# Optimization experiments

Hardware: AMD Instinct MI355X
Metric: run time of the kernel (lower is better)

Reference implementation:

```python
import jax, jax.numpy as jnp
import numpy as np

B, S, D, H = 2, 2048, 512, 8
HD = D // H  # head_size = 64
EPS = 1e-5


def _layer_norm(x, g, b):
    m = jnp.mean(x, axis=-1, keepdims=True)
    v = jnp.mean(jnp.square(x - m), axis=-1, keepdims=True)
    return (x - m) * jax.lax.rsqrt(v + EPS) * g + b


def setup_inputs() -> dict:
    key = jax.random.key(0)
    ks = jax.random.split(key, 16)
    s_in = 1.0 / np.sqrt(D)
    s_ff = 1.0 / np.sqrt(4 * D)
    return {
        "x": jax.random.normal(ks[0], (B, S, D), jnp.float32),
        # per-head q/k/v projections stacked over heads: [H, D, HD]
        "Wq": jax.random.normal(ks[1], (H, D, HD), jnp.float32) * s_in,
        "bq": jax.random.normal(ks[2], (H, HD), jnp.float32) * s_in,
        "Wk": jax.random.normal(ks[3], (H, D, HD), jnp.float32) * s_in,
        "bk": jax.random.normal(ks[4], (H, HD), jnp.float32) * s_in,
        "Wv": jax.random.normal(ks[5], (H, D, HD), jnp.float32) * s_in,
        "bv": jax.random.normal(ks[6], (H, HD), jnp.float32) * s_in,
        "Wp": jax.random.normal(ks[7], (D, D), jnp.float32) * s_in,
        "bp": jax.random.normal(ks[8], (D,), jnp.float32) * s_in,
        "W1": jax.random.normal(ks[9], (D, 4 * D), jnp.float32) * s_in,
        "b1": jax.random.normal(ks[10], (4 * D,), jnp.float32) * s_in,
        "W2": jax.random.normal(ks[11], (4 * D, D), jnp.float32) * s_ff,
        "b2": jax.random.normal(ks[12], (D,), jnp.float32) * s_ff,
        "g1": jnp.ones((D,), jnp.float32),
        "be1": jnp.zeros((D,), jnp.float32),
        "g2": jnp.ones((D,), jnp.float32),
        "be2": jnp.zeros((D,), jnp.float32),
    }


def reference(x, Wq, bq, Wk, bk, Wv, bv, Wp, bp, W1, b1, W2, b2, g1, be1, g2, be2):
    # --- attention sublayer (pre-norm) ---
    xn = _layer_norm(x, g1, be1)                               # [B,S,D]
    q = jnp.einsum('bsd,hde->bhse', xn, Wq) + bq[None, :, None, :]
    k = jnp.einsum('bsd,hde->bhse', xn, Wk) + bk[None, :, None, :]
    v = jnp.einsum('bsd,hde->bhse', xn, Wv) + bv[None, :, None, :]
    # NOTE: original has NO 1/sqrt(head_size) scaling and NO mask
    scores = jnp.einsum('bhse,bhte->bhst', q, k)               # [B,H,S,S]
    w = jax.nn.softmax(scores, axis=-1)
    o = jnp.einsum('bhst,bhte->bhse', w, v)                    # [B,H,S,HD]
    o = o.transpose(0, 2, 1, 3).reshape(x.shape[0], x.shape[1], D)  # concat heads
    attn_out = o @ Wp + bp
    x = x + attn_out
    # --- MLP sublayer (pre-norm) ---
    xn2 = _layer_norm(x, g2, be2)
    h = jax.nn.relu(xn2 @ W1 + b1)
    x = x + (h @ W2 + b2)
    return x
```

## Files before the change

kernel.cpp:

```cpp
#include <hip/hip_runtime.h>
#include <hip/hip_bf16.h>

typedef unsigned short u16;
typedef unsigned long long u64t;
typedef __attribute__((ext_vector_type(8))) short bhalf8;
typedef __attribute__((ext_vector_type(4))) short bhalf4;
typedef __attribute__((ext_vector_type(4))) float f32x4;

#define MFMA16(a, b, c) __builtin_amdgcn_mfma_f32_16x16x32_bf16((a), (b), (c), 0, 0, 0)

#if __has_builtin(__builtin_amdgcn_mfma_f32_16x16x16bf16_1k)
#define HAVE_K16 1
#define MFMAK16(a, b, c) __builtin_amdgcn_mfma_f32_16x16x16bf16_1k((a), (b), (c), 0, 0, 0)
#elif __has_builtin(__builtin_amdgcn_mfma_f32_16x16x16_bf16)
#define HAVE_K16 1
#define MFMAK16(a, b, c) __builtin_amdgcn_mfma_f32_16x16x16_bf16((a), (b), (c), 0, 0, 0)
#else
#define HAVE_K16 0
#endif

#if __has_builtin(__builtin_amdgcn_perm)
#define HAVE_PERM 1
#else
#define HAVE_PERM 0
#endif

#define BB 2
#define SS 2048
#define DD 512
#define HH 8
#define HD 64
#define NT (BB * SS)
#define LOG2E 1.44269504f

#if __has_builtin(__builtin_amdgcn_exp2f)
#define EXP2(x) __builtin_amdgcn_exp2f(x)
#else
#define EXP2(x) exp2f(x)
#endif

__device__ __forceinline__ u16 f2b(float f) {
    unsigned u = __builtin_bit_cast(unsigned, f);
    unsigned r = (u + 0x7fffu + ((u >> 16) & 1u)) >> 16;
    return (u16)r;
}

__device__ __forceinline__ unsigned pk2bf(float f0, float f1) {
#if HAVE_PERM
    unsigned a0 = __builtin_bit_cast(unsigned, f0) + 0x8000u;
    unsigned a1 = __builtin_bit_cast(unsigned, f1) + 0x8000u;
    return __builtin_amdgcn_perm(a1, a0, 0x07060302u);
#else
    return (unsigned)f2b(f0) | ((unsigned)f2b(f1) << 16);
#endif
}

__device__ __forceinline__ void gl2lds16(const u16* g, u16* l) {
    u16* gn = (u16*)g;
    __builtin_amdgcn_global_load_lds((__attribute__((address_space(1))) void*)gn,
                                     (__attribute__((address_space(3))) void*)l, 16, 0, 0);
}

__global__ __launch_bounds__(256) void k_prep(const float* __restrict__ Wq, const float* __restrict__ Wk,
                                              const float* __restrict__ Wv, const float* __restrict__ Wp,
                                              const float* __restrict__ W1, const float* __restrict__ W2,
                                              const float* __restrict__ bq, const float* __restrict__ bk,
                                              const float* __restrict__ bv,
                                              u16* __restrict__ WqkvT, u16* __restrict__ WpT,
                                              u16* __restrict__ W1T, u16* __restrict__ W2T,
                                              float* __restrict__ biasqkv,
                                              const float* __restrict__ x, const float* __restrict__ g1,
                                              const float* __restrict__ be1, u16* __restrict__ xn) {
    int j = blockIdx.x;
    int t = threadIdx.x;
    if (j >= 3078) {
        int wave = t >> 6, lane = t & 63;
        int row = (j - 3078) * 4 + wave;
        const float* xr = x + (size_t)row * DD;
        int c = lane * 8;
        float4 v0 = *(const float4*)(xr + c);
        float4 v1 = *(const float4*)(xr + c + 4);
        float s  = v0.x + v0.y + v0.z + v0.w + v1.x + v1.y + v1.z + v1.w;
        float sq = v0.x*v0.x + v0.y*v0.y + v0.z*v0.z + v0.w*v0.w
                 + v1.x*v1.x + v1.y*v1.y + v1.z*v1.z + v1.w*v1.w;
#pragma unroll
        for (int m = 1; m < 64; m <<= 1) {
            s  += __shfl_xor(s, m);
            sq += __shfl_xor(sq, m);
        }
        float mean = s * (1.0f / DD);
        float var  = sq * (1.0f / DD) - mean * mean;
        float rstd = rsqrtf(var + 1e-5f);
        float4 g0 = *(const float4*)(g1 + c);
        float4 g4 = *(const float4*)(g1 + c + 4);
        float4 b0 = *(const float4*)(be1 + c);
        float4 b4 = *(const float4*)(be1 + c + 4);
        float xv[8] = {v0.x, v0.y, v0.z, v0.w, v1.x, v1.y, v1.z, v1.w};
        float gv[8] = {g0.x, g0.y, g0.z, g0.w, g4.x, g4.y, g4.z, g4.w};
        float bv2[8] = {b0.x, b0.y, b0.z, b0.w, b4.x, b4.y, b4.z, b4.w};
        union { bhalf8 v; u16 u[8]; } pk;
#pragma unroll
        for (int i = 0; i < 8; i++) pk.u[i] = f2b((xv[i] - mean) * rstd * gv[i] + bv2[i]);
        *(bhalf8*)(xn + (size_t)row * DD + c) = pk.v;
        return;
    }
    int tx = t & 31, ty = t >> 5;
    if (j >= 3072) {
        int i = (j - 3072) * 256 + ty * 32 + tx;
        biasqkv[i] = (i < 512) ? bq[i] : (i < 1024) ? bk[i - 512] : bv[i - 1024];
        return;
    }
    __shared__ float tile[32][33];
    const float* src; u16* dst; int R, C, tr, tc;
    if (j < 768) {
        int m = j >> 8, rem = j & 255, h = rem >> 5, tl = rem & 31;
        tr = tl >> 1; tc = tl & 1;
        src = (m == 0 ? Wq : (m == 1 ? Wk : Wv)) + h * 32768;
        dst = WqkvT + m * 262144 + h * 32768;
        R = 512; C = 64;
    } else if (j < 1024) { int tl = j - 768;  tr = tl >> 4; tc = tl & 15; src = Wp; dst = WpT; R = 512;  C = 512;  }
    else if (j < 2048)   { int tl = j - 1024; tr = tl >> 6; tc = tl & 63; src = W1; dst = W1T; R = 512;  C = 2048; }
    else                 { int tl = j - 2048; tr = tl >> 4; tc = tl & 15; src = W2; dst = W2T; R = 2048; C = 512;  }
    int c = tc * 32 + tx;
#pragma unroll
    for (int i = 0; i < 4; i++)
        tile[ty + i * 8][tx] = src[(size_t)(tr * 32 + ty + i * 8) * C + c];
    __syncthreads();
    int r2 = tr * 32 + tx;
#pragma unroll
    for (int i = 0; i < 4; i++)
        dst[(size_t)(tc * 32 + ty + i * 8) * R + r2] = f2b(tile[tx][ty + i * 8]);
}

__global__ __launch_bounds__(256) void k_layernorm(const float* __restrict__ x,
                                                   const float* __restrict__ g,
                                                   const float* __restrict__ be,
                                                   u16* __restrict__ out) {
    int wave = threadIdx.x >> 6, lane = threadIdx.x & 63;
    int row = blockIdx.x * 4 + wave;
    const float* xr = x + (size_t)row * DD;
    int c = lane * 8;
    float4 v0 = *(const float4*)(xr + c);
    float4 v1 = *(const float4*)(xr + c + 4);
    float s  = v0.x + v0.y + v0.z + v0.w + v1.x + v1.y + v1.z + v1.w;
    float sq = v0.x*v0.x + v0.y*v0.y + v0.z*v0.z + v0.w*v0.w
             + v1.x*v1.x + v1.y*v1.y + v1.z*v1.z + v1.w*v1.w;
#pragma unroll
    for (int m = 1; m < 64; m <<= 1) {
        s  += __shfl_xor(s, m);
        sq += __shfl_xor(sq, m);
    }
    float mean = s * (1.0f / DD);
    float var  = sq * (1.0f / DD) - mean * mean;
    float rstd = rsqrtf(var + 1e-5f);
    float4 g0 = *(const float4*)(g + c);
    float4 g1 = *(const float4*)(g + c + 4);
    float4 b0 = *(const float4*)(be + c);
    float4 b1 = *(const float4*)(be + c + 4);
    float xv[8] = {v0.x, v0.y, v0.z, v0.w, v1.x, v1.y, v1.z, v1.w};
    float gv[8] = {g0.x, g0.y, g0.z, g0.w, g1.x, g1.y, g1.z, g1.w};
    float bv[8] = {b0.x, b0.y, b0.z, b0.w, b1.x, b1.y, b1.z, b1.w};
    union { bhalf8 v; u16 u[8]; } pk;
#pragma unroll
    for (int i = 0; i < 8; i++) pk.u[i] = f2b((xv[i] - mean) * rstd * gv[i] + bv[i]);
    *(bhalf8*)(out + (size_t)row * DD + c) = pk.v;
}

template<int BM, int BN, int WR, int WC, int MI, int NI, int MODE>
__global__ __launch_bounds__(256) void k_gemm(const u16* __restrict__ A, const u16* __restrict__ Bt,
                                              const float* __restrict__ bias,
                                              int lda, int ldb, int kLen, int N,
                                              const float* __restrict__ resid,
                                              float* __restrict__ outF, u16* __restrict__ outB,
                                              u16* __restrict__ qd, u16* __restrict__ kd,
                                              u16* __restrict__ vtd) {
    constexpr int WM = MI * 16;
    constexpr int WN = NI * 16;
    static_assert(WR * WM == BM && WC * WN == BN && WR * WC == 4, "cfg");
    constexpr int ACH = BM / 32;
    constexpr int BCH = BN / 32;
    __shared__ u16 As0[BM * 64];
    __shared__ u16 Bs0[BN * 64];
    __shared__ u16 As1[BM * 64];
    __shared__ u16 Bs1[BN * 64];
    int t = threadIdx.x;
    int wave = t >> 6, lane = t & 63, quad = lane >> 4, l16 = lane & 15;
    int wr, wc;
    if (WC == 1)      { wr = wave; wc = 0; }
    else if (WR == 1) { wr = 0;    wc = wave; }
    else              { wr = wave >> 1; wc = wave & 1; }
    int m0 = blockIdx.y * BM, n0 = blockIdx.x * BN;

    f32x4 acc[MI][NI] = {};

    int srow = lane >> 3;
    int scol = (lane & 7) * 8;
    const u16* Ag = A  + (size_t)(m0 + srow) * lda + scol;
    const u16* Bg = Bt + (size_t)(n0 + srow) * ldb + scol;

    auto stage = [&](u16* Asd, u16* Bsd, int k0) {
#pragma unroll
        for (int c = 0; c < ACH; c++) {
            int ch = wave * ACH + c;
            gl2lds16(Ag + (size_t)(ch * 8) * lda + k0, &Asd[ch * 512]);
        }
#pragma unroll
        for (int c = 0; c < BCH; c++) {
            int ch = wave * BCH + c;
            gl2lds16(Bg + (size_t)(ch * 8) * ldb + k0, &Bsd[ch * 512]);
        }
    };
    auto compute = [&](const u16* Asd, const u16* Bsd) {
#pragma unroll
        for (int h = 0; h < 2; h++) {
            bhalf8 af[MI], bf[NI];
#pragma unroll
            for (int mi = 0; mi < MI; mi++)
                af[mi] = *(const bhalf8*)&Asd[(wr * WM + mi * 16 + l16) * 64 + h * 32 + quad * 8];
#pragma unroll
            for (int ni = 0; ni < NI; ni++)
                bf[ni] = *(const bhalf8*)&Bsd[(wc * WN + ni * 16 + l16) * 64 + h * 32 + quad * 8];
#pragma unroll
            for (int mi = 0; mi < MI; mi++)
#pragma unroll
                for (int ni = 0; ni < NI; ni++)
                    acc[mi][ni] = MFMA16(af[mi], bf[ni], acc[mi][ni]);
        }
    };

    int nt = kLen >> 6;
    stage(As0, Bs0, 0);
    __syncthreads();
    for (int kt = 0; kt < nt; kt += 2) {
        if (kt + 1 < nt) stage(As1, Bs1, (kt + 1) << 6);
        compute(As0, Bs0);
        __syncthreads();
        if (kt + 1 < nt) {
            if (kt + 2 < nt) stage(As0, Bs0, (kt + 2) << 6);
            compute(As1, Bs1);
            __syncthreads();
        }
    }

#pragma unroll
    for (int mi = 0; mi < MI; mi++)
#pragma unroll
        for (int ni = 0; ni < NI; ni++) {
            f32x4 a = acc[mi][ni];
            int gc = n0 + wc * WN + ni * 16 + l16;
            int gr0 = m0 + wr * WM + mi * 16 + quad * 4;
            float bsv = bias[gc];
            if (MODE == 0) {
                int mm = gc >> 9, cc = gc & 511;
                int hh = cc >> 6, e = cc & 63;
                int b = gr0 >> 11, s0 = gr0 & 2047;
                if (mm == 2) {
                    u64t pk = 0;
#pragma unroll
                    for (int r = 0; r < 4; r++) pk |= (u64t)f2b(a[r] + bsv) << (16 * r);
                    *(u64t*)&vtd[((size_t)(b * HH + hh) * HD + e) * SS + s0] = pk;
                } else if (mm == 0) {
#pragma unroll
                    for (int r = 0; r < 4; r++)
                        qd[((size_t)(b * HH + hh) * SS + s0 + r) * HD + e] = f2b((a[r] + bsv) * LOG2E);
                } else {
#pragma unroll
                    for (int r = 0; r < 4; r++)
                        kd[((size_t)(b * HH + hh) * SS + s0 + r) * HD + e] = f2b(a[r] + bsv);
                }
            } else if (MODE == 1) {
#pragma unroll
                for (int r = 0; r < 4; r++) {
                    size_t idx = (size_t)(gr0 + r) * N + gc;
                    outF[idx] = a[r] + bsv + resid[idx];
                }
            } else {
#pragma unroll
                for (int r = 0; r < 4; r++)
                    outB[(size_t)(gr0 + r) * N + gc] = f2b(fmaxf(a[r] + bsv, 0.0f));
            }
        }
}

__global__ __launch_bounds__(512) void k_attention(const u16* __restrict__ q,
                                                   const u16* __restrict__ k,
                                                   const u16* __restrict__ vt,
                                                   float* __restrict__ Opart,
                                                   float* __restrict__ lsum) {
    __shared__ u16 sm[17920];
    u16* Ks = sm;
    u16* Vs = sm + 9216;
    float* Ored = (float*)sm;
    float* Lred = (float*)sm + 8192;

    int bh = blockIdx.x, qt = blockIdx.y, kspl = blockIdx.z;
    int t = threadIdx.x, wave = t >> 6, lane = t & 63, quad = lane >> 4, l16 = lane & 15;
    int g = wave >> 2, qw = wave & 3;
    const u16* qb = q  + (size_t)bh * SS * HD;
    const u16* kb = k  + (size_t)bh * SS * HD;
    const u16* vb = vt + (size_t)bh * HD * SS;

    bhalf8 qfa0, qfa1, qfb0, qfb1;
    {
        int r0 = qt * 128 + qw * 32 + l16;
        qfa0 = *(const bhalf8*)(qb + (size_t)r0 * HD + quad * 8);
        qfa1 = *(const bhalf8*)(qb + (size_t)r0 * HD + 32 + quad * 8);
        qfb0 = *(const bhalf8*)(qb + (size_t)(r0 + 16) * HD + quad * 8);
        qfb1 = *(const bhalf8*)(qb + (size_t)(r0 + 16) * HD + 32 + quad * 8);
    }

    f32x4 oacc[2][4] = {};
    f32x4 rsa4 = {}, rsb4 = {};

    int kr = t >> 2, kc = (t & 3) * 16;
    int vr = t >> 3, vc = (t & 7) * 16;
    const u16* kp = kb + ((size_t)kspl * 1024 + kr) * HD + kc;
    const u16* vp = vb + (size_t)vr * SS + kspl * 1024 + vc;
    u16* ksd = &Ks[kr * 72 + kc];
    u16* vsd = &Vs[vr * 136 + vc];

    bhalf8 kreg[2], vreg[2];
#pragma unroll
    for (int i = 0; i < 2; i++) {
        kreg[i] = *(const bhalf8*)(kp + i * 8);
        vreg[i] = *(const bhalf8*)(vp + i * 8);
    }

    for (int it = 0; it < 8; it++) {
        __syncthreads();
#pragma unroll
        for (int i = 0; i < 2; i++) {
            *(bhalf8*)(ksd + i * 8) = kreg[i];
            *(bhalf8*)(vsd + i * 8) = vreg[i];
        }
        __syncthreads();
        if (it < 7) {
            const u16* kn = kp + (size_t)(it + 1) * 128 * HD;
            const u16* vn = vp + (it + 1) * 128;
#pragma unroll
            for (int i = 0; i < 2; i++) {
                kreg[i] = *(const bhalf8*)(kn + i * 8);
                vreg[i] = *(const bhalf8*)(vn + i * 8);
            }
        }

#pragma unroll
        for (int nt2 = 0; nt2 < 4; nt2++) {
            int nt = g * 4 + nt2;
            bhalf8 kf0 = *(bhalf8*)&Ks[(nt * 16 + l16) * 72 + quad * 8];
            bhalf8 kf1 = *(bhalf8*)&Ks[(nt * 16 + l16) * 72 + 32 + quad * 8];
            f32x4 sa = {}, sb = {};
            __builtin_amdgcn_s_setprio(1);
            sa = MFMA16(kf0, qfa0, sa);
            sa = MFMA16(kf1, qfa1, sa);
            sb = MFMA16(kf0, qfb0, sb);
            sb = MFMA16(kf1, qfb1, sb);
            __builtin_amdgcn_s_setprio(0);
#if HAVE_K16
            float p0[4], p1[4];
#pragma unroll
            for (int r = 0; r < 4; r++) {
                p0[r] = EXP2(sa[r]);
                p1[r] = EXP2(sb[r]);
            }
#pragma unroll
            for (int r = 0; r < 4; r++) { rsa4[r] += p0[r]; rsb4[r] += p1[r]; }
            union { bhalf4 v; unsigned w[2]; } pa, pb;
            pa.w[0] = pk2bf(p0[0], p0[1]);
            pa.w[1] = pk2bf(p0[2], p0[3]);
            pb.w[0] = pk2bf(p1[0], p1[1]);
            pb.w[1] = pk2bf(p1[2], p1[3]);
            __builtin_amdgcn_s_setprio(1);
#pragma unroll
            for (int et = 0; et < 4; et++) {
                bhalf4 vf = *(bhalf4*)&Vs[(et * 16 + l16) * 136 + nt * 16 + quad * 4];
                oacc[0][et] = MFMAK16(pa.v, vf, oacc[0][et]);
                oacc[1][et] = MFMAK16(pb.v, vf, oacc[1][et]);
            }
            __builtin_amdgcn_s_setprio(0);
#else
            float p0[4], p1[4];
#pragma unroll
            for (int r = 0; r < 4; r++) {
                p0[r] = EXP2(sa[r]);
                p1[r] = EXP2(sb[r]);
                rsa4[r] += p0[r]; rsb4[r] += p1[r];
            }
            union { bhalf8 v; unsigned w[4]; } pa, pb;
            pa.w[0] = pk2bf(p0[0], p0[1]);
            pa.w[1] = pk2bf(p0[2], p0[3]);
            pa.w[2] = 0; pa.w[3] = 0;
            pb.w[0] = pk2bf(p1[0], p1[1]);
            pb.w[1] = pk2bf(p1[2], p1[3]);
            pb.w[2] = 0; pb.w[3] = 0;
            __builtin_amdgcn_s_setprio(1);
#pragma unroll
            for (int et = 0; et < 4; et++) {
                union { bhalf8 v; bhalf4 h[2]; } vf;
                vf.h[0] = *(bhalf4*)&Vs[(et * 16 + l16) * 136 + nt * 16 + quad * 4];
                vf.h[1] = (bhalf4){0, 0, 0, 0};
                oacc[0][et] = MFMA16(pa.v, vf.v, oacc[0][et]);
                oacc[1][et] = MFMA16(pb.v, vf.v, oacc[1][et]);
            }
            __builtin_amdgcn_s_setprio(0);
#endif
        }
    }

    float rsa = (rsa4[0] + rsa4[1]) + (rsa4[2] + rsa4[3]);
    float rsb = (rsb4[0] + rsb4[1]) + (rsb4[2] + rsb4[3]);
    rsa += __shfl_xor(rsa, 16); rsa += __shfl_xor(rsa, 32);
    rsb += __shfl_xor(rsb, 16); rsb += __shfl_xor(rsb, 32);

    __syncthreads();
    if (g == 1) {
#pragma unroll
        for (int qc = 0; qc < 2; qc++)
#pragma unroll
            for (int et = 0; et < 4; et++)
#pragma unroll
                for (int r = 0; r < 4; r++)
                    Ored[(qw * 32 + qc * 16 + quad * 4 + r) * 64 + et * 16 + l16] = oacc[qc][et][r];
        if (quad == 0) {
            Lred[qw * 32 + l16]      = rsa;
            Lred[qw * 32 + 16 + l16] = rsb;
        }
    }
    __syncthreads();
    if (g == 0) {
#pragma unroll
        for (int qc = 0; qc < 2; qc++) {
            int sbase = qt * 128 + qw * 32 + qc * 16;
            float* Ob = Opart + ((size_t)(kspl * 16 + bh) * SS + sbase) * HD;
#pragma unroll
            for (int et = 0; et < 4; et++)
#pragma unroll
                for (int r = 0; r < 4; r++) {
                    float v = oacc[qc][et][r]
                            + Ored[(qw * 32 + qc * 16 + quad * 4 + r) * 64 + et * 16 + l16];
                    Ob[(quad * 4 + r) * HD + et * 16 + l16] = v;
                }
            if (quad == 0)
                lsum[(size_t)(kspl * 16 + bh) * SS + sbase + l16] =
                    (qc == 0 ? rsa : rsb) + Lred[qw * 32 + qc * 16 + l16];
        }
    }
}

__global__ __launch_bounds__(256) void k_combine(const float* __restrict__ Opart,
                                                 const float* __restrict__ lsum,
                                                 u16* __restrict__ oc) {
    int tid = blockIdx.x * 256 + threadIdx.x;
    int c4 = tid & 15, s = (tid >> 4) & 2047, bh = tid >> 15;
    size_t i0 = ((size_t)bh * SS + s) * HD + c4 * 4;
    float4 p0 = *(const float4*)(Opart + i0);
    float4 p1 = *(const float4*)(Opart + (size_t)16 * SS * HD + i0);
    float l = lsum[(size_t)bh * SS + s] + lsum[(size_t)16 * SS + (size_t)bh * SS + s];
    float inv = 1.0f / l;
    u64t pk = 0;
    pk |= (u64t)f2b((p0.x + p1.x) * inv);
    pk |= (u64t)f2b((p0.y + p1.y) * inv) << 16;
    pk |= (u64t)f2b((p0.z + p1.z) * inv) << 32;
    pk |= (u64t)f2b((p0.w + p1.w) * inv) << 48;
    int b = bh >> 3, h = bh & 7;
    *(u64t*)&oc[((size_t)b * SS + s) * DD + h * HD + c4 * 4] = pk;
}

extern "C" void kernel_launch(void* const* d_in, const int* in_sizes, int n_in,
                              void* d_out, int out_size, void* d_ws, size_t ws_size,
                              hipStream_t stream) {
    const float* x   = (const float*)d_in[0];
    const float* Wq  = (const float*)d_in[1];
    const float* bq  = (const float*)d_in[2];
    const float* Wk  = (const float*)d_in[3];
    const float* bk  = (const float*)d_in[4];
    const float* Wv  = (const float*)d_in[5];
    const float* bv  = (const float*)d_in[6];
    const float* Wp  = (const float*)d_in[7];
    const float* bp  = (const float*)d_in[8];
    const float* W1  = (const float*)d_in[9];
    const float* b1  = (const float*)d_in[10];
    const float* W2  = (const float*)d_in[11];
    const float* b2  = (const float*)d_in[12];
    const float* g1  = (const float*)d_in[13];
    const float* be1 = (const float*)d_in[14];
    const float* g2  = (const float*)d_in[15];
    const float* be2 = (const float*)d_in[16];

    char* ws = (char*)d_ws;
    u16*   WqkvT   = (u16*)(ws + 0);
    u16*   WpT     = (u16*)(ws + 1572864);
    u16*   W1T     = (u16*)(ws + 2097152);
    u16*   W2T     = (u16*)(ws + 4194304);
    float* biasqkv = (float*)(ws + 6291456);
    u16*   xn      = (u16*)(ws + 6297600);
    u16*   qB      = (u16*)(ws + 10491904);
    u16*   kB      = (u16*)(ws + 14686208);
    u16*   vTb     = (u16*)(ws + 18880512);
    u16*   oc      = (u16*)(ws + 23074816);
    float* x1      = (float*)(ws + 27269120);
    u16*   xn2     = (u16*)(ws + 35657728);
    u16*   hbuf    = (u16*)(ws + 39852032);
    float* Opart   = (float*)hbuf;
    float* lsum    = (float*)xn;

    k_prep<<<4102, 256, 0, stream>>>(Wq, Wk, Wv, Wp, W1, W2, bq, bk, bv,
                                     WqkvT, WpT, W1T, W2T, biasqkv,
                                     x, g1, be1, xn);
    k_gemm<128, 128, 2, 2, 4, 4, 0><<<dim3(12, 32), 256, 0, stream>>>(
        xn, WqkvT, biasqkv, 512, 512, 512, 1536, nullptr, nullptr, nullptr, qB, kB, vTb);
    k_attention<<<dim3(16, 16, 2), 512, 0, stream>>>(qB, kB, vTb, Opart, lsum);
    k_combine<<<2048, 256, 0, stream>>>(Opart, lsum, oc);
    k_gemm<64, 64, 2, 2, 2, 2, 1><<<dim3(8, 64), 256, 0, stream>>>(
        oc, WpT, bp, 512, 512, 512, 512, x, x1, nullptr, nullptr, nullptr, nullptr);
    k_layernorm<<<NT / 4, 256, 0, stream>>>(x1, g2, be2, xn2);
    k_gemm<128, 128, 2, 2, 4, 4, 2><<<dim3(16, 32), 256, 0, stream>>>(
        xn2, W1T, b1, 512, 512, 512, 2048, nullptr, nullptr, hbuf, nullptr, nullptr, nullptr);
    k_gemm<64, 64, 2, 2, 2, 2, 1><<<dim3(8, 64), 256, 0, stream>>>(
        hbuf, W2T, b2, 2048, 2048, 2048, 512, x1, (float*)d_out, nullptr, nullptr, nullptr, nullptr);
}
```

Measured before the change: 199.6 us.

## Double-buffer K/V tiles in LDS for attention kernel

Switches the attention kernel's K/V shared-memory staging from a single buffer to two ping-pong buffers. Global loads for the next tile are stored into the alternate buffer while the current tile is being computed, cutting barriers from two per tile to one. This doubles LDS usage per block, which may reduce how many blocks fit on a CU.

```diff
diff --git a/kernel.cpp b/kernel.cpp
--- a/kernel.cpp
+++ b/kernel.cpp
@@ -287,9 +287,11 @@
                                                    const u16* __restrict__ vt,
                                                    float* __restrict__ Opart,
                                                    float* __restrict__ lsum) {
-    __shared__ u16 sm[17920];
-    u16* Ks = sm;
-    u16* Vs = sm + 9216;
+    __shared__ u16 sm[35840];
+    u16* Ks0 = sm;
+    u16* Vs0 = sm + 9216;
+    u16* Ks1 = sm + 17920;
+    u16* Vs1 = sm + 27136;
     float* Ored = (float*)sm;
     float* Lred = (float*)sm + 8192;
 
@@ -316,8 +318,8 @@
     int vr = t >> 3, vc = (t & 7) * 16;
     const u16* kp = kb + ((size_t)kspl * 1024 + kr) * HD + kc;
     const u16* vp = vb + (size_t)vr * SS + kspl * 1024 + vc;
-    u16* ksd = &Ks[kr * 72 + kc];
-    u16* vsd = &Vs[vr * 136 + vc];
+    int koff = kr * 72 + kc;
+    int voff = vr * 136 + vc;
 
     bhalf8 kreg[2], vreg[2];
 #pragma unroll
@@ -325,30 +327,24 @@
         kreg[i] = *(const bhalf8*)(kp + i * 8);
         vreg[i] = *(const bhalf8*)(vp + i * 8);
     }
-
-    for (int it = 0; it < 8; it++) {
-        __syncthreads();
-#pragma unroll
-        for (int i = 0; i < 2; i++) {
-            *(bhalf8*)(ksd + i * 8) = kreg[i];
-            *(bhalf8*)(vsd + i * 8) = vreg[i];
-        }
-        __syncthreads();
-        if (it < 7) {
-            const u16* kn = kp + (size_t)(it + 1) * 128 * HD;
-            const u16* vn = vp + (it + 1) * 128;
-#pragma unroll
-            for (int i = 0; i < 2; i++) {
-                kreg[i] = *(const bhalf8*)(kn + i * 8);
-                vreg[i] = *(const bhalf8*)(vn + i * 8);
-            }
-        }
-
+#pragma unroll
+    for (int i = 0; i < 2; i++) {
+        *(bhalf8*)(&Ks0[koff] + i * 8) = kreg[i];
+        *(bhalf8*)(&Vs0[voff] + i * 8) = vreg[i];
+    }
+    __syncthreads();
+#pragma unroll
+    for (int i = 0; i < 2; i++) {
+        kreg[i] = *(const bhalf8*)(kp + (size_t)128 * HD + i * 8);
+        vreg[i] = *(const bhalf8*)(vp + 128 + i * 8);
+    }
+
+    auto att_step = [&](const u16* Ksb, const u16* Vsb) {
 #pragma unroll
         for (int nt2 = 0; nt2 < 4; nt2++) {
             int nt = g * 4 + nt2;
-            bhalf8 kf0 = *(bhalf8*)&Ks[(nt * 16 + l16) * 72 + quad * 8];
-            bhalf8 kf1 = *(bhalf8*)&Ks[(nt * 16 + l16) * 72 + 32 + quad * 8];
+            bhalf8 kf0 = *(const bhalf8*)&Ksb[(nt * 16 + l16) * 72 + quad * 8];
+            bhalf8 kf1 = *(const bhalf8*)&Ksb[(nt * 16 + l16) * 72 + 32 + quad * 8];
             f32x4 sa = {}, sb = {};
             __builtin_amdgcn_s_setprio(1);
             sa = MFMA16(kf0, qfa0, sa);
@@ -373,7 +369,7 @@
             __builtin_amdgcn_s_setprio(1);
 #pragma unroll
             for (int et = 0; et < 4; et++) {
-                bhalf4 vf = *(bhalf4*)&Vs[(et * 16 + l16) * 136 + nt * 16 + quad * 4];
+                bhalf4 vf = *(const bhalf4*)&Vsb[(et * 16 + l16) * 136 + nt * 16 + quad * 4];
                 oacc[0][et] = MFMAK16(pa.v, vf, oacc[0][et]);
                 oacc[1][et] = MFMAK16(pb.v, vf, oacc[1][et]);
             }
@@ -397,7 +393,7 @@
 #pragma unroll
             for (int et = 0; et < 4; et++) {
                 union { bhalf8 v; bhalf4 h[2]; } vf;
-                vf.h[0] = *(bhalf4*)&Vs[(et * 16 + l16) * 136 + nt * 16 + quad * 4];
+                vf.h[0] = *(const bhalf4*)&Vsb[(et * 16 + l16) * 136 + nt * 16 + quad * 4];
                 vf.h[1] = (bhalf4){0, 0, 0, 0};
                 oacc[0][et] = MFMA16(pa.v, vf.v, oacc[0][et]);
                 oacc[1][et] = MFMA16(pb.v, vf.v, oacc[1][et]);
@@ -405,6 +401,43 @@
             __builtin_amdgcn_s_setprio(0);
 #endif
         }
+    };
+
+    for (int it = 0; it < 8; it += 2) {
+#pragma unroll
+        for (int i = 0; i < 2; i++) {
+            *(bhalf8*)(&Ks1[koff] + i * 8) = kreg[i];
+            *(bhalf8*)(&Vs1[voff] + i * 8) = vreg[i];
+        }
+        if (it + 2 < 8) {
+            const u16* kn = kp + (size_t)(it + 2) * 128 * HD;
+            const u16* vn = vp + (it + 2) * 128;
+#pragma unroll
+            for (int i = 0; i < 2; i++) {
+                kreg[i] = *(const bhalf8*)(kn + i * 8);
+                vreg[i] = *(const bhalf8*)(vn + i * 8);
+            }
+        }
+        att_step(Ks0, Vs0);
+        __syncthreads();
+        if (it + 2 < 8) {
+#pragma unroll
+            for (int i = 0; i < 2; i++) {
+                *(bhalf8*)(&Ks0[koff] + i * 8) = kreg[i];
+                *(bhalf8*)(&Vs0[voff] + i * 8) = vreg[i];
+            }
+            if (it + 3 < 8) {
+                const u16* kn = kp + (size_t)(it + 3) * 128 * HD;
+                const u16* vn = vp + (it + 3) * 128;
+#pragma unroll
+                for (int i = 0; i < 2; i++) {
+                    kreg[i] = *(const bhalf8*)(kn + i * 8);
+                    vreg[i] = *(const bhalf8*)(vn + i * 8);
+                }
+            }
+        }
+        att_step(Ks1, Vs1);
+        __syncthreads();
     }
 
     float rsa = (rsa4[0] + rsa4[1]) + (rsa4[2] + rsa4[3]);
@@ -412,7 +445,6 @@
     rsa += __shfl_xor(rsa, 16); rsa += __shfl_xor(rsa, 32);
     rsb += __shfl_xor(rsb, 16); rsb += __shfl_xor(rsb, 32);
 
-    __syncthreads();
     if (g == 1) {
 #pragma unroll
         for (int qc = 0; qc < 2; qc++)
```

Result: no change. 199.8 us (+0.1%).
